# Kernel optimization log

Measured on AMD Instinct MI355X. Metric: run time of the kernel, lower is better.

## Reference

```python
import jax, jax.numpy as jnp
import numpy as np

B, T, C, H, E, K, F = 2, 2048, 1024, 16, 8, 2, 2048  # batch, seq, d_model, heads, experts, top_k, d_ffn
EPS = 1e-5


def setup_inputs() -> dict:
    key = jax.random.key(0)
    ks = jax.random.split(key, 6)
    s = 0.02
    return {
        "x": jax.random.normal(ks[0], (B, T, C), jnp.float32),
        "ln1_w": jnp.ones((C,), jnp.float32),
        "c_attn_w": jax.random.normal(ks[1], (C, 3 * C), jnp.float32) * s,
        "c_proj_w": jax.random.normal(ks[2], (C, C), jnp.float32) * s,
        "ln2_w": jnp.ones((C,), jnp.float32),
        "router_w": jax.random.normal(ks[3], (C, E), jnp.float32) * s,
        "w1": jnp.clip(jax.random.normal(ks[4], (C, E * F), jnp.float32) * s, -0.06, 0.06),
        "w2": jnp.clip(jax.random.normal(ks[5], (E * F, C), jnp.float32) * s, -0.06, 0.06),
    }


def layernorm(x, w):
    m = x.mean(-1, keepdims=True)
    v = x.var(-1, keepdims=True)
    return (x - m) * jax.lax.rsqrt(v + EPS) * w


def attention(x, c_attn_w, c_proj_w):
    b, t, c = x.shape
    hd = c // H
    q, k, v = jnp.split(x @ c_attn_w, 3, axis=-1)
    q = q.reshape(b, t, H, hd).transpose(0, 2, 1, 3)  # bhtd
    k = k.reshape(b, t, H, hd).transpose(0, 2, 1, 3)
    v = v.reshape(b, t, H, hd).transpose(0, 2, 1, 3)
    att = jnp.einsum('bhqd,bhkd->bhqk', q, k) / jnp.sqrt(jnp.asarray(hd, x.dtype))
    causal = jnp.tril(jnp.ones((t, t), bool))
    att = jnp.where(causal, att, jnp.asarray(-jnp.inf, att.dtype))
    att = jax.nn.softmax(att, axis=-1)
    y = jnp.einsum('bhqk,bhkd->bhqd', att, v)
    y = y.transpose(0, 2, 1, 3).reshape(b, t, c)
    return y @ c_proj_w


def moe_mlp(x, router_w, w1, w2):
    b, t, c = x.shape
    xf = x.reshape(-1, c)  # (N, C), N = b*t
    router_logits = xf @ router_w  # (N, E)
    probs = jax.nn.softmax(router_logits.astype(jnp.float32), axis=-1)
    rw, sel = jax.lax.top_k(probs, K)  # (N, K)
    rw = rw / rw.sum(axis=-1, keepdims=True)  # norm_topk_prob=True
    rw = rw.astype(x.dtype)
    # expert e uses w1[:, e*F:(e+1)*F] and w2[e*F:(e+1)*F, :]
    w1e = w1.reshape(c, E, F).transpose(1, 0, 2)  # (E, C, F)
    w2e = w2.reshape(E, F, c)  # (E, F, C)
    h = jax.nn.gelu(jnp.einsum('nc,ecf->enf', xf, w1e), approximate=False)
    y_all = jnp.einsum('enf,efc->nec', h, w2e)  # (N, E, C)
    y_sel = jnp.take_along_axis(y_all, sel[:, :, None], axis=1)  # (N, K, C)
    y = (y_sel * rw[:, :, None]).sum(axis=1)
    return y.reshape(b, t, c)


def reference(x, ln1_w, c_attn_w, c_proj_w, ln2_w, router_w, w1, w2):
    x = x + attention(layernorm(x, ln1_w), c_attn_w, c_proj_w)
    x = x + moe_mlp(layernorm(x, ln2_w), router_w, w1, w2)
    return x
```

## Files before the change

kernel.cpp:

```cpp
#include <hip/hip_runtime.h>
#include <hip/hip_bf16.h>

#define BB 2
#define TT 2048
#define CCH 1024
#define HH 16
#define HD 64
#define EE 8
#define FF 2048
#define NTOK (BB*TT)

typedef __bf16 bf16x8 __attribute__((ext_vector_type(8)));
typedef float f32x4 __attribute__((ext_vector_type(4)));
typedef unsigned int u32;
typedef const u32 __attribute__((address_space(1)))* gads;
typedef u32 __attribute__((address_space(3)))* lads;

static __device__ __forceinline__ unsigned short f2bf(float f) {
  union { float f; unsigned u; } v; v.f = f;
  unsigned u = v.u;
  u += 0x7fffu + ((u >> 16) & 1u);
  return (unsigned short)(u >> 16);
}
static __device__ __forceinline__ float bf2f(unsigned short h) {
  union { unsigned u; float f; } v; v.u = ((unsigned)h) << 16;
  return v.f;
}

__global__ __launch_bounds__(256) void k_transpose(const float* __restrict__ in,
    unsigned short* __restrict__ out, int R, int Cc) {
  __shared__ float tile[32][33];
  size_t zoff = (size_t)blockIdx.z * (size_t)R * (size_t)Cc;
  int r0 = blockIdx.y * 32, c0 = blockIdx.x * 32;
  int tx = threadIdx.x, ty = threadIdx.y;
#pragma unroll
  for (int ii = 0; ii < 4; ++ii) {
    int i = ty + ii * 8;
    tile[i][tx] = in[zoff + (size_t)(r0 + i) * Cc + c0 + tx];
  }
  __syncthreads();
#pragma unroll
  for (int ii = 0; ii < 4; ++ii) {
    int i = ty + ii * 8;
    out[zoff + (size_t)(c0 + i) * R + r0 + tx] = f2bf(tile[tx][i]);
  }
}

__global__ __launch_bounds__(256) void k_ln(const float* __restrict__ x,
    const float* __restrict__ w, unsigned short* __restrict__ out) {
  int row = blockIdx.x;
  const float* xr = x + (size_t)row * CCH;
  int tid = threadIdx.x;
  float4 v = *(const float4*)&xr[tid * 4];
  float s = v.x + v.y + v.z + v.w;
  float ss = v.x * v.x + v.y * v.y + v.z * v.z + v.w * v.w;
#pragma unroll
  for (int off = 32; off; off >>= 1) { s += __shfl_xor(s, off); ss += __shfl_xor(ss, off); }
  __shared__ float red[8];
  int wv = tid >> 6, l = tid & 63;
  if (l == 0) { red[wv] = s; red[4 + wv] = ss; }
  __syncthreads();
  s = red[0] + red[1] + red[2] + red[3];
  ss = red[4] + red[5] + red[6] + red[7];
  float mean = s * (1.f / CCH);
  float var = ss * (1.f / CCH) - mean * mean;
  float inv = rsqrtf(var + 1e-5f);
  float4 w4 = *(const float4*)&w[tid * 4];
  ushort4 o;
  o.x = f2bf((v.x - mean) * inv * w4.x);
  o.y = f2bf((v.y - mean) * inv * w4.y);
  o.z = f2bf((v.z - mean) * inv * w4.z);
  o.w = f2bf((v.w - mean) * inv * w4.w);
  *(ushort4*)&out[(size_t)row * CCH + tid * 4] = o;
}

__global__ __launch_bounds__(256) void k_ln2_router(const float* __restrict__ x,
    const float* __restrict__ w, const float* __restrict__ rw,
    unsigned short* __restrict__ out, int* __restrict__ sel,
    float* __restrict__ selw) {
  int row = blockIdx.x;
  const float* xr = x + (size_t)row * CCH;
  int tid = threadIdx.x;
  float4 v = *(const float4*)&xr[tid * 4];
  float s = v.x + v.y + v.z + v.w;
  float ss = v.x * v.x + v.y * v.y + v.z * v.z + v.w * v.w;
#pragma unroll
  for (int off = 32; off; off >>= 1) { s += __shfl_xor(s, off); ss += __shfl_xor(ss, off); }
  __shared__ float red[8];
  __shared__ float red2[4][8];
  int wv = tid >> 6, l = tid & 63;
  if (l == 0) { red[wv] = s; red[4 + wv] = ss; }
  __syncthreads();
  s = red[0] + red[1] + red[2] + red[3];
  ss = red[4] + red[5] + red[6] + red[7];
  float mean = s * (1.f / CCH);
  float var = ss * (1.f / CCH) - mean * mean;
  float inv = rsqrtf(var + 1e-5f);
  float4 w4 = *(const float4*)&w[tid * 4];
  float nv0 = (v.x - mean) * inv * w4.x;
  float nv1 = (v.y - mean) * inv * w4.y;
  float nv2 = (v.z - mean) * inv * w4.z;
  float nv3 = (v.w - mean) * inv * w4.w;
  ushort4 o;
  o.x = f2bf(nv0); o.y = f2bf(nv1); o.z = f2bf(nv2); o.w = f2bf(nv3);
  *(ushort4*)&out[(size_t)row * CCH + tid * 4] = o;
  const float* rr = rw + (size_t)tid * 4 * EE;
  float lg[8];
#pragma unroll
  for (int e = 0; e < 8; ++e)
    lg[e] = nv0 * rr[e] + nv1 * rr[8 + e] + nv2 * rr[16 + e] + nv3 * rr[24 + e];
#pragma unroll
  for (int e = 0; e < 8; ++e) {
    float t = lg[e];
#pragma unroll
    for (int off = 32; off; off >>= 1) t += __shfl_xor(t, off);
    lg[e] = t;
  }
  if (l == 0) {
#pragma unroll
    for (int e = 0; e < 8; ++e) red2[wv][e] = lg[e];
  }
  __syncthreads();
  if (tid == 0) {
    float logit[8];
#pragma unroll
    for (int e = 0; e < 8; ++e)
      logit[e] = red2[0][e] + red2[1][e] + red2[2][e] + red2[3][e];
    float m1 = logit[0]; int i1 = 0;
#pragma unroll
    for (int e = 1; e < 8; ++e) if (logit[e] > m1) { m1 = logit[e]; i1 = e; }
    float m2 = -INFINITY; int i2 = 0;
#pragma unroll
    for (int e = 0; e < 8; ++e) if (e != i1 && logit[e] > m2) { m2 = logit[e]; i2 = e; }
    float w1v = 1.f / (1.f + __expf(m2 - m1));
    sel[row * 2] = i1; sel[row * 2 + 1] = i2;
    selw[row * 2] = w1v; selw[row * 2 + 1] = 1.f - w1v;
  }
}

#define CSP 140
#define CFP 70
template<int EPI>
__global__ __launch_bounds__(256, 4) void k_gemm128(
    const unsigned short* __restrict__ A, const unsigned short* __restrict__ BT,
    unsigned short* __restrict__ Cb, float* __restrict__ Cf,
    const float* __restrict__ resid, int M, int N, int K,
    const int* __restrict__ tokarr, const int* __restrict__ slotarr,
    const float* __restrict__ wgtarr, const int* __restrict__ offs,
    const int* __restrict__ counts, const int* __restrict__ tmap)
{
  __shared__ __align__(16) char pool[35840];
  unsigned short* As = (unsigned short*)pool;
  unsigned short* Bs = (unsigned short*)(pool + 16384);

  int mb, nb, e = 0, off = 0, cnt = M;
  if (EPI >= 2) {
    int tm = blockIdx.x;
    if (tm >= tmap[8]) return;
    e = 0;
    while (tm >= tmap[e + 1]) ++e;
    mb = tm - tmap[e];
    nb = blockIdx.y;
    cnt = counts[e]; off = offs[e];
  } else {
    int gx = gridDim.x, gy = gridDim.y;
    int nwg = gx * gy;
    int orig = blockIdx.y * gx + blockIdx.x;
    int q = nwg >> 3, r = nwg & 7;
    int xcd = orig & 7, idx = orig >> 3;
    int wk = (xcd < r ? xcd * (q + 1) : r * (q + 1) + (xcd - r) * q) + idx;
    nb = wk % gy; mb = wk / gy;
  }
  int m0 = mb * 128, n0 = nb * 128;

  int tid = threadIdx.x, l = tid & 63, w = tid >> 6;
  int scol = (((l & 7) ^ ((l >> 3) & 7)) * 8);
  const unsigned short* aptr[4];
  const unsigned short* bptr[4];
  const unsigned short* bbase = BT + (size_t)e * (size_t)N * K;
#pragma unroll
  for (int i = 0; i < 4; ++i) {
    int row = (w * 4 + i) * 8 + (l >> 3);
    int ra;
    if (EPI == 2)      ra = tokarr[off + min(m0 + row, cnt - 1)];
    else if (EPI == 3) ra = off + min(m0 + row, cnt - 1);
    else               ra = m0 + row;
    aptr[i] = A + (size_t)ra * K + scol;
    bptr[i] = bbase + (size_t)(n0 + row) * K + scol;
  }

  int wr = (w >> 1) * 64, wc = (w & 1) * 64;
  int frow = l & 15;
  int fkB = (l >> 4) * 16;
  int swz = (frow & 7) << 4;
  f32x4 acc[4][4] = {};

  for (int k0 = 0; k0 < K; k0 += 64) {
#pragma unroll
    for (int i = 0; i < 4; ++i) {
      int j = w * 4 + i;
      __builtin_amdgcn_global_load_lds((gads)(const void*)(aptr[i] + k0),
                                       (lads)(void*)(As + j * 512), 16, 0, 0);
      __builtin_amdgcn_global_load_lds((gads)(const void*)(bptr[i] + k0),
                                       (lads)(void*)(Bs + j * 512), 16, 0, 0);
    }
    __syncthreads();
    const char* ab = (const char*)As;
    const char* bb = (const char*)Bs;
#pragma unroll
    for (int kk = 0; kk < 2; ++kk) {
      int inr = (kk * 64 + fkB) ^ swz;
      bf16x8 af[4], bfr[4];
#pragma unroll
      for (int mi = 0; mi < 4; ++mi)
        af[mi] = *(const bf16x8*)(ab + (wr + mi * 16 + frow) * 128 + inr);
#pragma unroll
      for (int ni = 0; ni < 4; ++ni)
        bfr[ni] = *(const bf16x8*)(bb + (wc + ni * 16 + frow) * 128 + inr);
#pragma unroll
      for (int mi = 0; mi < 4; ++mi)
#pragma unroll
        for (int ni = 0; ni < 4; ++ni)
          acc[mi][ni] = __builtin_amdgcn_mfma_f32_16x16x32_bf16(af[mi], bfr[ni],
                                                                acc[mi][ni], 0, 0, 0);
    }
    __syncthreads();
  }

  int g4 = (l >> 4) * 4, cl = l & 15;

  if (EPI == 0 || EPI == 2) {
    unsigned short* Cs = (unsigned short*)pool;
#pragma unroll
    for (int mi = 0; mi < 4; ++mi)
#pragma unroll
      for (int ni = 0; ni < 4; ++ni)
#pragma unroll
        for (int r2 = 0; r2 < 4; ++r2) {
          float v = acc[mi][ni][r2];
          if (EPI == 2) v = 0.5f * v * (1.f + erff(v * 0.70710678118654752f));
          Cs[(wr + mi * 16 + g4 + r2) * CSP + wc + ni * 16 + cl] = f2bf(v);
        }
    __syncthreads();
    int row = tid >> 1, c0 = (tid & 1) * 64;
    if (EPI == 0 || m0 + row < cnt) {
      size_t grow = (EPI == 2) ? (size_t)(off + m0 + row) : (size_t)(m0 + row);
      unsigned short* dst = Cb + grow * N + n0 + c0;
#pragma unroll
      for (int j = 0; j < 8; ++j)
        ((uint4*)dst)[j] = *(const uint4*)&Cs[row * CSP + c0 + j * 8];
    }
  } else {
    float* Csf = (float*)pool;
#pragma unroll
    for (int p = 0; p < 2; ++p) {
      __syncthreads();
      if ((w & 1) == p) {
#pragma unroll
        for (int mi = 0; mi < 4; ++mi)
#pragma unroll
          for (int ni = 0; ni < 4; ++ni)
#pragma unroll
            for (int r2 = 0; r2 < 4; ++r2)
              Csf[(wr + mi * 16 + g4 + r2) * CFP + ni * 16 + cl] = acc[mi][ni][r2];
      }
      __syncthreads();
      int row = tid >> 1, c0 = (tid & 1) * 32;
      int gcol = n0 + p * 64 + c0;
      if (EPI == 1) {
        float* dst = Cf + (size_t)(m0 + row) * N + gcol;
        const float* rsd = resid + (size_t)(m0 + row) * N + gcol;
#pragma unroll
        for (int j = 0; j < 8; ++j) {
          float4 v = *(const float4*)&Csf[row * CFP + c0 + j * 4];
          float4 rr = ((const float4*)rsd)[j];
          v.x += rr.x; v.y += rr.y; v.z += rr.z; v.w += rr.w;
          ((float4*)dst)[j] = v;
        }
      } else {
        if (m0 + row < cnt) {
          int fl = off + m0 + row;
          int tok = tokarr[fl], slot = slotarr[fl];
          float wg = wgtarr[fl];
          float* dst = Cf + ((size_t)tok * 2 + slot) * N + gcol;
#pragma unroll
          for (int j = 0; j < 8; ++j) {
            float4 v = *(const float4*)&Csf[row * CFP + c0 + j * 4];
            v.x *= wg; v.y *= wg; v.z *= wg; v.w *= wg;
            ((float4*)dst)[j] = v;
          }
        }
      }
    }
  }
}

__global__ __launch_bounds__(256) void k_attn_mfma(const unsigned short* __restrict__ qkv,
    unsigned short* __restrict__ yout)
{
  int fblk = blockIdx.x;
  int xcd = fblk & 7, s = fblk >> 3;
  int hb = s & 3;
  int h = xcd + 8 * (hb & 1);
  int b = hb >> 1;
  int t = s >> 2, t0 = t & 7, u = t >> 3;
  int qt = (u == 0) ? t0 : (u == 1) ? (15 - t0) : (u == 2) ? (16 + t0) : (31 - t0);
  int q0 = qt * 64;

  int tid = threadIdx.x, l = tid & 63, w = tid >> 6;
  const size_t rs = 3 * CCH;

  __shared__ __align__(16) unsigned short Ks[64][72];
  __shared__ __align__(16) unsigned short VtL[64 * 72];
  __shared__ __align__(16) unsigned short Ps[4][16][72];

  int frow = l & 15, fk = (l >> 4) * 8;
  int g4 = l >> 4;
  int kr = tid >> 2, kc0 = (tid & 3) * 8;
  int vr = tid >> 2, vc0 = (tid & 3) * 16;
  int vphys = (((vr >> 3) + 2 * (tid & 3)) & 7) * 8 + (vr & 7);

  const unsigned short* qp = qkv + (size_t)((size_t)b * TT + q0 + w * 16 + frow) * rs + h * HD;
  bf16x8 qf0 = *(const bf16x8*)&qp[fk];
  bf16x8 qf1 = *(const bf16x8*)&qp[32 + fk];

  f32x4 oacc[4] = {};
  float mrow[4] = {-INFINITY, -INFINITY, -INFINITY, -INFINITY};
  float lrow[4] = {};

  uint4 rk0, rk1, rv0, rv1;
  {
    const unsigned short* kp = qkv + (size_t)((size_t)b * TT + kr) * rs + CCH + h * HD;
    rk0 = *(const uint4*)&kp[kc0];
    rk1 = *(const uint4*)&kp[kc0 + 32];
    const unsigned short* vp = qkv + (size_t)((size_t)b * TT + vr) * rs + 2 * CCH + h * HD + vc0;
    rv0 = *(const uint4*)&vp[0];
    rv1 = *(const uint4*)&vp[8];
  }

  for (int kb = 0; kb <= qt; ++kb) {
    __syncthreads();
    *(uint4*)&Ks[kr][kc0]      = rk0;
    *(uint4*)&Ks[kr][kc0 + 32] = rk1;
    {
      unsigned short tmp[16];
      *(uint4*)&tmp[0] = rv0; *(uint4*)&tmp[8] = rv1;
#pragma unroll
      for (int j = 0; j < 16; ++j) VtL[(vc0 + j) * 72 + vphys] = tmp[j];
    }
    __syncthreads();
    if (kb < qt) {
      int k0n = (kb + 1) * 64;
      const unsigned short* kp = qkv + (size_t)((size_t)b * TT + k0n + kr) * rs + CCH + h * HD;
      rk0 = *(const uint4*)&kp[kc0];
      rk1 = *(const uint4*)&kp[kc0 + 32];
      const unsigned short* vp = qkv + (size_t)((size_t)b * TT + k0n + vr) * rs + 2 * CCH + h * HD + vc0;
      rv0 = *(const uint4*)&vp[0];
      rv1 = *(const uint4*)&vp[8];
    }

    f32x4 sacc[4] = {};
#pragma unroll
    for (int nb = 0; nb < 4; ++nb) {
      bf16x8 kf0 = *(const bf16x8*)&Ks[nb * 16 + frow][fk];
      bf16x8 kf1 = *(const bf16x8*)&Ks[nb * 16 + frow][32 + fk];
      sacc[nb] = __builtin_amdgcn_mfma_f32_16x16x32_bf16(qf0, kf0, sacc[nb], 0, 0, 0);
      sacc[nb] = __builtin_amdgcn_mfma_f32_16x16x32_bf16(qf1, kf1, sacc[nb], 0, 0, 0);
    }

    bool diag = (kb == qt);
    float sv[4][4];
#pragma unroll
    for (int nb = 0; nb < 4; ++nb)
#pragma unroll
      for (int r = 0; r < 4; ++r) {
        float v = sacc[nb][r] * 0.125f;
        if (diag) {
          int ckv = nb * 16 + frow;
          int rq = w * 16 + 4 * g4 + r;
          if (ckv > rq) v = -INFINITY;
        }
        sv[nb][r] = v;
      }
    float fscale[4];
#pragma unroll
    for (int r = 0; r < 4; ++r) {
      float vm = fmaxf(fmaxf(sv[0][r], sv[1][r]), fmaxf(sv[2][r], sv[3][r]));
      vm = fmaxf(vm, __shfl_xor(vm, 1));
      vm = fmaxf(vm, __shfl_xor(vm, 2));
      vm = fmaxf(vm, __shfl_xor(vm, 4));
      vm = fmaxf(vm, __shfl_xor(vm, 8));
      float mnew = fmaxf(mrow[r], vm);
      float f = __expf(mrow[r] - mnew);
      mrow[r] = mnew;
      fscale[r] = f;
      float psum = 0.f;
#pragma unroll
      for (int nb = 0; nb < 4; ++nb) {
        float p = __expf(sv[nb][r] - mnew);
        sv[nb][r] = p;
        psum += p;
      }
      psum += __shfl_xor(psum, 1);
      psum += __shfl_xor(psum, 2);
      psum += __shfl_xor(psum, 4);
      psum += __shfl_xor(psum, 8);
      lrow[r] = lrow[r] * f + psum;
    }
#pragma unroll
    for (int nb = 0; nb < 4; ++nb)
#pragma unroll
      for (int r = 0; r < 4; ++r) {
        oacc[nb][r] *= fscale[r];
        Ps[w][4 * g4 + r][nb * 16 + frow] = f2bf(sv[nb][r]);
      }
#pragma unroll
    for (int ks = 0; ks < 2; ++ks) {
      bf16x8 pa = *(const bf16x8*)&Ps[w][frow][ks * 32 + fk];
#pragma unroll
      for (int nb = 0; nb < 4; ++nb) {
        int vchunk = ((ks * 4 + (l >> 4) + 2 * nb) & 7) * 8;
        bf16x8 vb = *(const bf16x8*)&VtL[(nb * 16 + frow) * 72 + vchunk];
        oacc[nb] = __builtin_amdgcn_mfma_f32_16x16x32_bf16(pa, vb, oacc[nb], 0, 0, 0);
      }
    }
  }

  unsigned short* yo = yout + (size_t)((size_t)b * TT + q0 + w * 16) * CCH + h * HD;
#pragma unroll
  for (int r = 0; r < 4; ++r) {
    float inv = 1.f / lrow[r];
    int row = 4 * g4 + r;
#pragma unroll
    for (int nb = 0; nb < 4; ++nb)
      yo[(size_t)row * CCH + nb * 16 + frow] = f2bf(oacc[nb][r] * inv);
  }
}

__global__ __launch_bounds__(256) void k_count(const int* __restrict__ sel,
    int* __restrict__ counts_pad)
{
  __shared__ int hist[8];
  int tid = threadIdx.x;
  if (tid < 8) hist[tid] = 0;
  __syncthreads();
  int i = blockIdx.x * 256 + tid;
  atomicAdd(&hist[sel[i]], 1);
  __syncthreads();
  if (tid < 8) atomicAdd(&counts_pad[tid * 16], hist[tid]);
}

__global__ void k_offsets(const int* __restrict__ counts_pad, int* __restrict__ counts,
                          int* __restrict__ offs, int* __restrict__ cursors_pad,
                          int* __restrict__ tmap) {
  if (threadIdx.x == 0 && blockIdx.x == 0) {
    int acc = 0, t = 0;
    tmap[0] = 0;
    for (int e = 0; e < 8; ++e) {
      int c = counts_pad[e * 16];
      counts[e] = c; offs[e] = acc; cursors_pad[e * 16] = acc; acc += c;
      t += (c + 127) >> 7;
      tmap[e + 1] = t;
    }
  }
}

__global__ __launch_bounds__(256) void k_scatter(const int* __restrict__ sel,
    const float* __restrict__ selw, int* __restrict__ cursors_pad,
    int* __restrict__ tokarr, int* __restrict__ slotarr, float* __restrict__ wgtarr)
{
  int t = blockIdx.x * 256 + threadIdx.x;
  int l = threadIdx.x & 63;
#pragma unroll
  for (int s2 = 0; s2 < 2; ++s2) {
    int e = sel[t * 2 + s2];
    int pos = 0;
#pragma unroll
    for (int ex = 0; ex < 8; ++ex) {
      unsigned long long mask = __ballot(e == ex);
      if (e == ex) {
        int leader = __ffsll((long long)mask) - 1;
        int cntw = __popcll(mask);
        int base = 0;
        if (l == leader) base = atomicAdd(&cursors_pad[ex * 16], cntw);
        base = __shfl(base, leader);
        unsigned long long below = (l == 0) ? 0ull : (mask << (64 - l));
        pos = base + __popcll(below);
      }
    }
    tokarr[pos] = t; slotarr[pos] = s2; wgtarr[pos] = selw[t * 2 + s2];
  }
}

__global__ __launch_bounds__(256) void k_combine(const float* __restrict__ x2,
    const float* __restrict__ yp, float* __restrict__ out)
{
  int i = blockIdx.x * 256 + threadIdx.x;
  int n = i >> 8, cw = i & 255;
  float4 a = ((const float4*)x2)[i];
  float4 y0 = ((const float4*)yp)[(size_t)(n * 2) * 256 + cw];
  float4 y1 = ((const float4*)yp)[(size_t)(n * 2 + 1) * 256 + cw];
  float4 o;
  o.x = a.x + y0.x + y1.x;
  o.y = a.y + y0.y + y1.y;
  o.z = a.z + y0.z + y1.z;
  o.w = a.w + y0.w + y1.w;
  ((float4*)out)[i] = o;
}

extern "C" void kernel_launch(void* const* d_in, const int* in_sizes, int n_in,
                              void* d_out, int out_size, void* d_ws, size_t ws_size,
                              hipStream_t stream) {
  const float* x     = (const float*)d_in[0];
  const float* ln1w  = (const float*)d_in[1];
  const float* attnw = (const float*)d_in[2];
  const float* projw = (const float*)d_in[3];
  const float* ln2w  = (const float*)d_in[4];
  const float* routw = (const float*)d_in[5];
  const float* w1    = (const float*)d_in[6];
  const float* w2    = (const float*)d_in[7];
  char* ws = (char*)d_ws;

  unsigned short* attn_wT = (unsigned short*)(ws + 0);
  unsigned short* proj_wT = (unsigned short*)(ws + 6291456);
  unsigned short* w1T     = (unsigned short*)(ws + 8388608);
  unsigned short* w2T     = (unsigned short*)(ws + 41943040);
  unsigned short* xn      = (unsigned short*)(ws + 75497472);
  unsigned short* qkv     = (unsigned short*)(ws + 83886080);
  unsigned short* yattn   = (unsigned short*)(ws + 109051904);
  unsigned short* hbuf    = (unsigned short*)(ws + 83886080);
  float* x2 = (float*)(ws + 117440512);
  float* yp = (float*)(ws + 134217728);
  char* rbase = ws + 167772160;
  int* counts_pad  = (int*)(rbase);
  int* counts      = (int*)(rbase + 512);
  int* cursors_pad = (int*)(rbase + 1024);
  int* offs        = (int*)(rbase + 1536);
  int* tmap        = (int*)(rbase + 1600);
  int* sel         = (int*)(rbase + 2048);
  float* selw      = (float*)(rbase + 2048 + 32768);
  int* tokarr      = (int*)(rbase + 2048 + 65536);
  int* slotarr     = (int*)(rbase + 2048 + 98304);
  float* wgtarr    = (float*)(rbase + 2048 + 131072);
  float* outp = (float*)d_out;

  hipMemsetAsync(counts_pad, 0, 512, stream);

  dim3 tb(32, 8);
  k_transpose<<<dim3(96, 32, 1), tb, 0, stream>>>(attnw, attn_wT, 1024, 3072);
  k_transpose<<<dim3(32, 32, 1), tb, 0, stream>>>(projw, proj_wT, 1024, 1024);
  k_transpose<<<dim3(512, 32, 1), tb, 0, stream>>>(w1, w1T, 1024, 16384);
  k_transpose<<<dim3(32, 64, 8), tb, 0, stream>>>(w2, w2T, 2048, 1024);

  k_ln<<<NTOK, 256, 0, stream>>>(x, ln1w, xn);
  k_gemm128<0><<<dim3(32, 24), 256, 0, stream>>>(xn, attn_wT, qkv, nullptr, nullptr,
      NTOK, 3 * CCH, CCH, nullptr, nullptr, nullptr, nullptr, nullptr, nullptr);
  k_attn_mfma<<<dim3(1024), 256, 0, stream>>>(qkv, yattn);
  k_gemm128<1><<<dim3(32, 8), 256, 0, stream>>>(yattn, proj_wT, nullptr, x2, x,
      NTOK, CCH, CCH, nullptr, nullptr, nullptr, nullptr, nullptr, nullptr);
  k_ln2_router<<<NTOK, 256, 0, stream>>>(x2, ln2w, routw, xn, sel, selw);
  k_count<<<32, 256, 0, stream>>>(sel, counts_pad);
  k_offsets<<<1, 64, 0, stream>>>(counts_pad, counts, offs, cursors_pad, tmap);
  k_scatter<<<NTOK / 256, 256, 0, stream>>>(sel, selw, cursors_pad, tokarr, slotarr, wgtarr);
  k_gemm128<2><<<dim3(72, 16), 256, 0, stream>>>(xn, w1T, hbuf, nullptr, nullptr,
      NTOK, FF, CCH, tokarr, slotarr, wgtarr, offs, counts, tmap);
  k_gemm128<3><<<dim3(72, 8), 256, 0, stream>>>(hbuf, w2T, nullptr, yp, nullptr,
      NTOK, CCH, FF, tokarr, slotarr, wgtarr, offs, counts, tmap);
  k_combine<<<4096, 256, 0, stream>>>(x2, yp, outp);
}
```

Measured before the change: 389.2 us.

## Use tanh-GELU, bf16 expert outputs, and MFMA priority hints in attention

The exact erf GELU in the first expert GEMM epilogue is replaced by the tanh approximation, computed with a single exp. The second expert GEMM now writes its weighted per-slot outputs as bf16 through the shared-memory staging path instead of fp32, and the combine kernel reads bf16, which halves that intermediate traffic. The attention kernel wraps its MFMA blocks in s_setprio to favour matrix issue across waves. The tanh approximation and the bf16 rounding of expert outputs add numerical error relative to the exact reference.

```diff
diff --git a/kernel.cpp b/kernel.cpp
--- a/kernel.cpp
+++ b/kernel.cpp
@@ -229,7 +229,7 @@
 
   int g4 = (l >> 4) * 4, cl = l & 15;
 
-  if (EPI == 0 || EPI == 2) {
+  if (EPI == 0 || EPI == 2 || EPI == 3) {
     unsigned short* Cs = (unsigned short*)pool;
 #pragma unroll
     for (int mi = 0; mi < 4; ++mi)
@@ -238,17 +238,40 @@
 #pragma unroll
         for (int r2 = 0; r2 < 4; ++r2) {
           float v = acc[mi][ni][r2];
-          if (EPI == 2) v = 0.5f * v * (1.f + erff(v * 0.70710678118654752f));
+          if (EPI == 2) {
+            float u2 = 1.5957691216f * v * (1.f + 0.044715f * v * v);
+            float ex = __expf(u2);
+            v = v - v / (ex + 1.f);
+          }
           Cs[(wr + mi * 16 + g4 + r2) * CSP + wc + ni * 16 + cl] = f2bf(v);
         }
     __syncthreads();
     int row = tid >> 1, c0 = (tid & 1) * 64;
     if (EPI == 0 || m0 + row < cnt) {
-      size_t grow = (EPI == 2) ? (size_t)(off + m0 + row) : (size_t)(m0 + row);
-      unsigned short* dst = Cb + grow * N + n0 + c0;
-#pragma unroll
-      for (int j = 0; j < 8; ++j)
-        ((uint4*)dst)[j] = *(const uint4*)&Cs[row * CSP + c0 + j * 8];
+      if (EPI == 3) {
+        int fl = off + m0 + row;
+        int tok = tokarr[fl], slot = slotarr[fl];
+        float wg = wgtarr[fl];
+        unsigned short* dst = Cb + ((size_t)tok * 2 + slot) * N + n0 + c0;
+#pragma unroll
+        for (int j = 0; j < 8; ++j) {
+          uint4 pk = *(const uint4*)&Cs[row * CSP + c0 + j * 8];
+          unsigned short* sp = (unsigned short*)&pk;
+          ushort4 o0, o1;
+          o0.x = f2bf(bf2f(sp[0]) * wg); o0.y = f2bf(bf2f(sp[1]) * wg);
+          o0.z = f2bf(bf2f(sp[2]) * wg); o0.w = f2bf(bf2f(sp[3]) * wg);
+          o1.x = f2bf(bf2f(sp[4]) * wg); o1.y = f2bf(bf2f(sp[5]) * wg);
+          o1.z = f2bf(bf2f(sp[6]) * wg); o1.w = f2bf(bf2f(sp[7]) * wg);
+          *(ushort4*)&dst[j * 8] = o0;
+          *(ushort4*)&dst[j * 8 + 4] = o1;
+        }
+      } else {
+        size_t grow = (EPI == 2) ? (size_t)(off + m0 + row) : (size_t)(m0 + row);
+        unsigned short* dst = Cb + grow * N + n0 + c0;
+#pragma unroll
+        for (int j = 0; j < 8; ++j)
+          ((uint4*)dst)[j] = *(const uint4*)&Cs[row * CSP + c0 + j * 8];
+      }
     }
   } else {
     float* Csf = (float*)pool;
@@ -267,29 +290,14 @@
       __syncthreads();
       int row = tid >> 1, c0 = (tid & 1) * 32;
       int gcol = n0 + p * 64 + c0;
-      if (EPI == 1) {
-        float* dst = Cf + (size_t)(m0 + row) * N + gcol;
-        const float* rsd = resid + (size_t)(m0 + row) * N + gcol;
-#pragma unroll
-        for (int j = 0; j < 8; ++j) {
-          float4 v = *(const float4*)&Csf[row * CFP + c0 + j * 4];
-          float4 rr = ((const float4*)rsd)[j];
-          v.x += rr.x; v.y += rr.y; v.z += rr.z; v.w += rr.w;
-          ((float4*)dst)[j] = v;
-        }
-      } else {
-        if (m0 + row < cnt) {
-          int fl = off + m0 + row;
-          int tok = tokarr[fl], slot = slotarr[fl];
-          float wg = wgtarr[fl];
-          float* dst = Cf + ((size_t)tok * 2 + slot) * N + gcol;
-#pragma unroll
-          for (int j = 0; j < 8; ++j) {
-            float4 v = *(const float4*)&Csf[row * CFP + c0 + j * 4];
-            v.x *= wg; v.y *= wg; v.z *= wg; v.w *= wg;
-            ((float4*)dst)[j] = v;
-          }
-        }
+      float* dst = Cf + (size_t)(m0 + row) * N + gcol;
+      const float* rsd = resid + (size_t)(m0 + row) * N + gcol;
+#pragma unroll
+      for (int j = 0; j < 8; ++j) {
+        float4 v = *(const float4*)&Csf[row * CFP + c0 + j * 4];
+        float4 rr = ((const float4*)rsd)[j];
+        v.x += rr.x; v.y += rr.y; v.z += rr.z; v.w += rr.w;
+        ((float4*)dst)[j] = v;
       }
     }
   }
@@ -360,6 +368,7 @@
     }
 
     f32x4 sacc[4] = {};
+    __builtin_amdgcn_s_setprio(1);
 #pragma unroll
     for (int nb = 0; nb < 4; ++nb) {
       bf16x8 kf0 = *(const bf16x8*)&Ks[nb * 16 + frow][fk];
@@ -367,6 +376,7 @@
       sacc[nb] = __builtin_amdgcn_mfma_f32_16x16x32_bf16(qf0, kf0, sacc[nb], 0, 0, 0);
       sacc[nb] = __builtin_amdgcn_mfma_f32_16x16x32_bf16(qf1, kf1, sacc[nb], 0, 0, 0);
     }
+    __builtin_amdgcn_s_setprio(0);
 
     bool diag = (kb == qt);
     float sv[4][4];
@@ -414,6 +424,7 @@
         oacc[nb][r] *= fscale[r];
         Ps[w][4 * g4 + r][nb * 16 + frow] = f2bf(sv[nb][r]);
       }
+    __builtin_amdgcn_s_setprio(1);
 #pragma unroll
     for (int ks = 0; ks < 2; ++ks) {
       bf16x8 pa = *(const bf16x8*)&Ps[w][frow][ks * 32 + fk];
@@ -424,6 +435,7 @@
         oacc[nb] = __builtin_amdgcn_mfma_f32_16x16x32_bf16(pa, vb, oacc[nb], 0, 0, 0);
       }
     }
+    __builtin_amdgcn_s_setprio(0);
   }
 
   unsigned short* yo = yout + (size_t)((size_t)b * TT + q0 + w * 16) * CCH + h * HD;
@@ -493,19 +505,27 @@
 }
 
 __global__ __launch_bounds__(256) void k_combine(const float* __restrict__ x2,
-    const float* __restrict__ yp, float* __restrict__ out)
+    const unsigned short* __restrict__ ypb, float* __restrict__ out)
 {
   int i = blockIdx.x * 256 + threadIdx.x;
-  int n = i >> 8, cw = i & 255;
-  float4 a = ((const float4*)x2)[i];
-  float4 y0 = ((const float4*)yp)[(size_t)(n * 2) * 256 + cw];
-  float4 y1 = ((const float4*)yp)[(size_t)(n * 2 + 1) * 256 + cw];
-  float4 o;
-  o.x = a.x + y0.x + y1.x;
-  o.y = a.y + y0.y + y1.y;
-  o.z = a.z + y0.z + y1.z;
-  o.w = a.w + y0.w + y1.w;
-  ((float4*)out)[i] = o;
+  int n = i >> 7, cw = i & 127;
+  float4 a0 = ((const float4*)x2)[i * 2];
+  float4 a1 = ((const float4*)x2)[i * 2 + 1];
+  uint4 y0p = *(const uint4*)&ypb[((size_t)n * 2) * CCH + cw * 8];
+  uint4 y1p = *(const uint4*)&ypb[((size_t)n * 2 + 1) * CCH + cw * 8];
+  const unsigned short* y0 = (const unsigned short*)&y0p;
+  const unsigned short* y1 = (const unsigned short*)&y1p;
+  float4 o0, o1;
+  o0.x = a0.x + bf2f(y0[0]) + bf2f(y1[0]);
+  o0.y = a0.y + bf2f(y0[1]) + bf2f(y1[1]);
+  o0.z = a0.z + bf2f(y0[2]) + bf2f(y1[2]);
+  o0.w = a0.w + bf2f(y0[3]) + bf2f(y1[3]);
+  o1.x = a1.x + bf2f(y0[4]) + bf2f(y1[4]);
+  o1.y = a1.y + bf2f(y0[5]) + bf2f(y1[5]);
+  o1.z = a1.z + bf2f(y0[6]) + bf2f(y1[6]);
+  o1.w = a1.w + bf2f(y0[7]) + bf2f(y1[7]);
+  ((float4*)out)[i * 2] = o0;
+  ((float4*)out)[i * 2 + 1] = o1;
 }
 
 extern "C" void kernel_launch(void* const* d_in, const int* in_sizes, int n_in,
@@ -530,7 +550,7 @@
   unsigned short* yattn   = (unsigned short*)(ws + 109051904);
   unsigned short* hbuf    = (unsigned short*)(ws + 83886080);
   float* x2 = (float*)(ws + 117440512);
-  float* yp = (float*)(ws + 134217728);
+  unsigned short* ypb = (unsigned short*)(ws + 134217728);
   char* rbase = ws + 167772160;
   int* counts_pad  = (int*)(rbase);
   int* counts      = (int*)(rbase + 512);
@@ -564,7 +584,7 @@
   k_scatter<<<NTOK / 256, 256, 0, stream>>>(sel, selw, cursors_pad, tokarr, slotarr, wgtarr);
   k_gemm128<2><<<dim3(72, 16), 256, 0, stream>>>(xn, w1T, hbuf, nullptr, nullptr,
       NTOK, FF, CCH, tokarr, slotarr, wgtarr, offs, counts, tmap);
-  k_gemm128<3><<<dim3(72, 8), 256, 0, stream>>>(hbuf, w2T, nullptr, yp, nullptr,
+  k_gemm128<3><<<dim3(72, 8), 256, 0, stream>>>(hbuf, w2T, ypb, nullptr, nullptr,
       NTOK, CCH, FF, tokarr, slotarr, wgtarr, offs, counts, tmap);
-  k_combine<<<4096, 256, 0, stream>>>(x2, yp, outp);
-}
+  k_combine<<<2048, 256, 0, stream>>>(x2, ypb, outp);
+}
```

After: 379.1 us. -2.6%, faster.
